# Performance work log

Measured on AMD Instinct MI355X. Metric: run time of the kernel, lower is better.

## Reference

```python
import jax, jax.numpy as jnp
import numpy as np

B, S, H, E, NF, NM = 4096, 512, 5, 4, 1, 64  # batch, seq, hidden, embed_dim, numeric feats, num_mote_ids
D = NF + E  # lstm input size = 5


def setup_inputs() -> dict:
    key = jax.random.key(0)
    k = jax.random.split(key, 7)
    s = 1.0 / np.sqrt(H)  # PyTorch LSTM init scale
    return {
        "x_num": jax.random.normal(k[0], (B, S, NF), jnp.float32),
        "x_cat": jax.random.randint(k[1], (B, S, 1), 0, NM, jnp.int32),
        "embed": jax.random.normal(k[2], (NM, E), jnp.float32),
        "W_ih": jax.random.uniform(k[3], (4 * H, D), jnp.float32, -s, s),
        "W_hh": jax.random.uniform(k[4], (4 * H, H), jnp.float32, -s, s),
        "b_ih": jax.random.uniform(k[5], (4 * H,), jnp.float32, -s, s),
        "b_hh": jax.random.uniform(k[6], (4 * H,), jnp.float32, -s, s),
    }


def reference(x_num, x_cat, embed, W_ih, W_hh, b_ih, b_hh):
    # embedding lookup + concat -> [B, S, D]
    emb = embed[x_cat[:, :, 0]]
    x = jnp.concatenate([x_num, emb], axis=2)
    # precompute input-to-gate projections once: [B, S, 4H]
    xg = jnp.einsum('bsd,gd->bsg', x, W_ih) + b_ih + b_hh

    def step(carry, xt):  # xt: [B, 4H]
        h, c = carry
        g = xt + h @ W_hh.T
        i, f, gg, o = jnp.split(g, 4, axis=-1)  # PyTorch gate order: i, f, g, o
        i = jax.nn.sigmoid(i)
        f = jax.nn.sigmoid(f)
        gg = jnp.tanh(gg)
        o = jax.nn.sigmoid(o)
        c = f * c + i * gg
        h = o * jnp.tanh(c)
        return (h, c), h

    h0 = jnp.zeros((B, H), x.dtype)
    c0 = jnp.zeros((B, H), x.dtype)
    (hT, cT), outs = jax.lax.scan(step, (h0, c0), jnp.swapaxes(xg, 0, 1))
    out = jnp.swapaxes(outs, 0, 1)  # [B, S, H]
    return out, hT[None], cT[None]  # hidden/cell: [num_layers=1, B, H]
```

## Files before the change

kernel.cpp:

```cpp
#include <hip/hip_runtime.h>

#define NBATCH 4096
#define SEQ 512
#define HID 5
#define NEMB 64

__device__ __forceinline__ float fexp2(float x){ return __builtin_amdgcn_exp2f(x); }
__device__ __forceinline__ float frcp(float x){ return __builtin_amdgcn_rcpf(x); }

#define SWZ(v, k) __int_as_float(__builtin_amdgcn_ds_swizzle(__float_as_int(v), ((4*(k)) << 5)))
#define DPPQ(v, j) __int_as_float(__builtin_amdgcn_update_dpp(0, __float_as_int(v), ((j) * 0x55), 0xF, 0xF, true))

__global__ __launch_bounds__(64) void lstm_enc_kernel(
    const float* __restrict__ x_num, const int* __restrict__ x_cat,
    const float* __restrict__ embed, const float* __restrict__ W_ih,
    const float* __restrict__ W_hh, const float* __restrict__ b_ih,
    const float* __restrict__ b_hh, float* __restrict__ out)
{
    __shared__ float4 s_emb[NEMB];
    int tid = threadIdx.x;
    s_emb[tid] = ((const float4*)embed)[tid];
    __syncthreads();

    int half = tid >> 5;
    int l    = tid & 31;
    int b    = blockIdx.x * 2 + half;
    int k    = ((l >> 2) < HID) ? (l >> 2) : (HID - 1);
    int g    = l & 3;
    bool st  = (l < 20) && (g == 0);

    const float L2E = 1.4426950408889634f;
    float s_  = (g == 2) ? (-2.0f * L2E) : (-L2E);
    float fm  = (g == 2) ? 2.0f : 1.0f;
    float fb  = (g == 2) ? -1.0f : 0.0f;

    int row = g * HID + k;
    float wi_[5], wh_[5];
#pragma unroll
    for (int d = 0; d < 5; ++d) {
        wi_[d] = W_ih[row * 5 + d] * s_;
        wh_[d] = W_hh[row * 5 + d] * s_;
    }
    float bias = (b_ih[row] + b_hh[row]) * s_;

    const float4* xp = (const float4*)(x_num + (size_t)b * SEQ);
    const int4*   cp = (const int4*)(x_cat + (size_t)b * SEQ);
    float* outp = out + (size_t)b * SEQ * HID + k;

    float h = 0.f, c = 0.f;
    float hb0 = 0.f, hb1 = 0.f, hb2 = 0.f, hb3 = 0.f, hb4 = 0.f;

    float4 xf = xp[0];
    int4   cf = cp[0];
    float4 ec_[4];
    ec_[0] = s_emb[cf.x]; ec_[1] = s_emb[cf.y];
    ec_[2] = s_emb[cf.z]; ec_[3] = s_emb[cf.w];

    for (int t0 = 0; t0 < SEQ; t0 += 4) {
        int nidx = (t0 + 4 < SEQ) ? ((t0 >> 2) + 1) : 0;
        float4 xf_n = xp[nidx];
        int4   cf_n = cp[nidx];

        float xn_a[4] = {xf.x, xf.y, xf.z, xf.w};

        float xa[4];
#pragma unroll
        for (int u = 0; u < 4; ++u) {
            float4 e = ec_[u];
            float a = fmaf(xn_a[u], wi_[0], bias);
            a = fmaf(e.x, wi_[1], a);
            a = fmaf(e.y, wi_[2], a);
            a = fmaf(e.z, wi_[3], a);
            a = fmaf(e.w, wi_[4], a);
            xa[u] = a;
        }

#pragma unroll
        for (int u = 0; u < 4; ++u) {
            float a = xa[u];
            a = fmaf(hb0, wh_[0], a);
            a = fmaf(hb1, wh_[1], a);
            a = fmaf(hb2, wh_[2], a);
            a = fmaf(hb3, wh_[3], a);
            a = fmaf(hb4, wh_[4], a);

            float r = frcp(1.0f + fexp2(a));
            float v = fmaf(r, fm, fb);

            float ai = DPPQ(v, 0);
            float af = DPPQ(v, 1);
            float ag = DPPQ(v, 2);
            float ao = DPPQ(v, 3);

            c = fmaf(af, c, ai * ag);
            float tc = fmaf(frcp(1.0f + fexp2(c * (-2.0f * L2E))), 2.0f, -1.0f);
            h = ao * tc;

            hb0 = SWZ(h, 0);
            hb1 = SWZ(h, 1);
            hb2 = SWZ(h, 2);
            hb3 = SWZ(h, 3);
            hb4 = SWZ(h, 4);

            if (st) outp[(t0 + u) * HID] = h;
        }

        ec_[0] = s_emb[cf_n.x]; ec_[1] = s_emb[cf_n.y];
        ec_[2] = s_emb[cf_n.z]; ec_[3] = s_emb[cf_n.w];
        xf = xf_n;
    }

    if (st) {
        size_t base = (size_t)NBATCH * SEQ * HID;
        out[base + (size_t)b * HID + k] = h;
        out[base + (size_t)NBATCH * HID + (size_t)b * HID + k] = c;
    }
}

extern "C" void kernel_launch(void* const* d_in, const int* in_sizes, int n_in,
                              void* d_out, int out_size, void* d_ws, size_t ws_size,
                              hipStream_t stream) {
    const float* x_num = (const float*)d_in[0];
    const int*   x_cat = (const int*)d_in[1];
    const float* embed = (const float*)d_in[2];
    const float* W_ih  = (const float*)d_in[3];
    const float* W_hh  = (const float*)d_in[4];
    const float* b_ih  = (const float*)d_in[5];
    const float* b_hh  = (const float*)d_in[6];
    float* out = (float*)d_out;

    dim3 grid(NBATCH / 2);
    dim3 block(64);
    hipLaunchKernelGGL(lstm_enc_kernel, grid, block, 0, stream,
                       x_num, x_cat, embed, W_ih, W_hh, b_ih, b_hh, out);
}
```

Before: 89.44 us.

## Interleave two independent batch recurrences per thread and halve the grid

Each wavefront now processes four batch sequences, two per half-wave, by running two independent LSTM recurrences interleaved in the same thread. The intent is to expose instruction-level parallelism across the latency-bound serial chain of cross-lane ops and exp/rcp, instead of relying on multiple waves per SIMD. The grid is halved, which reduces the number of resident waves, and register use roughly doubles.

After: 130.3 us. 1.46x slower.

```diff
diff --git a/kernel.cpp b/kernel.cpp
--- a/kernel.cpp
+++ b/kernel.cpp
@@ -24,7 +24,8 @@
 
     int half = tid >> 5;
     int l    = tid & 31;
-    int b    = blockIdx.x * 2 + half;
+    int bA   = blockIdx.x * 4 + half;
+    int bB   = bA + 2;
     int k    = ((l >> 2) < HID) ? (l >> 2) : (HID - 1);
     int g    = l & 3;
     bool st  = (l < 20) && (g == 0);
@@ -43,77 +44,111 @@
     }
     float bias = (b_ih[row] + b_hh[row]) * s_;
 
-    const float4* xp = (const float4*)(x_num + (size_t)b * SEQ);
-    const int4*   cp = (const int4*)(x_cat + (size_t)b * SEQ);
-    float* outp = out + (size_t)b * SEQ * HID + k;
+    const float4* xpA = (const float4*)(x_num + (size_t)bA * SEQ);
+    const int4*   cpA = (const int4*)(x_cat + (size_t)bA * SEQ);
+    float* outpA = out + (size_t)bA * SEQ * HID + k;
+    const float4* xpB = (const float4*)(x_num + (size_t)bB * SEQ);
+    const int4*   cpB = (const int4*)(x_cat + (size_t)bB * SEQ);
+    float* outpB = out + (size_t)bB * SEQ * HID + k;
 
-    float h = 0.f, c = 0.f;
-    float hb0 = 0.f, hb1 = 0.f, hb2 = 0.f, hb3 = 0.f, hb4 = 0.f;
+    float hA = 0.f, cA = 0.f, hB = 0.f, cB = 0.f;
+    float hbA0 = 0.f, hbA1 = 0.f, hbA2 = 0.f, hbA3 = 0.f, hbA4 = 0.f;
+    float hbB0 = 0.f, hbB1 = 0.f, hbB2 = 0.f, hbB3 = 0.f, hbB4 = 0.f;
 
-    float4 xf = xp[0];
-    int4   cf = cp[0];
-    float4 ec_[4];
-    ec_[0] = s_emb[cf.x]; ec_[1] = s_emb[cf.y];
-    ec_[2] = s_emb[cf.z]; ec_[3] = s_emb[cf.w];
+    float4 xfA = xpA[0];  int4 cfA = cpA[0];
+    float4 xfB = xpB[0];  int4 cfB = cpB[0];
+    float4 ecA_[4], ecB_[4];
+    ecA_[0] = s_emb[cfA.x]; ecA_[1] = s_emb[cfA.y]; ecA_[2] = s_emb[cfA.z]; ecA_[3] = s_emb[cfA.w];
+    ecB_[0] = s_emb[cfB.x]; ecB_[1] = s_emb[cfB.y]; ecB_[2] = s_emb[cfB.z]; ecB_[3] = s_emb[cfB.w];
 
     for (int t0 = 0; t0 < SEQ; t0 += 4) {
         int nidx = (t0 + 4 < SEQ) ? ((t0 >> 2) + 1) : 0;
-        float4 xf_n = xp[nidx];
-        int4   cf_n = cp[nidx];
+        float4 xfA_n = xpA[nidx];  int4 cfA_n = cpA[nidx];
+        float4 xfB_n = xpB[nidx];  int4 cfB_n = cpB[nidx];
 
-        float xn_a[4] = {xf.x, xf.y, xf.z, xf.w};
+        float xnA[4] = {xfA.x, xfA.y, xfA.z, xfA.w};
+        float xnB[4] = {xfB.x, xfB.y, xfB.z, xfB.w};
 
-        float xa[4];
+        float xaA[4], xaB[4];
 #pragma unroll
         for (int u = 0; u < 4; ++u) {
-            float4 e = ec_[u];
-            float a = fmaf(xn_a[u], wi_[0], bias);
-            a = fmaf(e.x, wi_[1], a);
-            a = fmaf(e.y, wi_[2], a);
-            a = fmaf(e.z, wi_[3], a);
-            a = fmaf(e.w, wi_[4], a);
-            xa[u] = a;
+            float4 eA = ecA_[u];
+            float a = fmaf(xnA[u], wi_[0], bias);
+            a = fmaf(eA.x, wi_[1], a);
+            a = fmaf(eA.y, wi_[2], a);
+            a = fmaf(eA.z, wi_[3], a);
+            a = fmaf(eA.w, wi_[4], a);
+            xaA[u] = a;
+            float4 eB = ecB_[u];
+            float bx = fmaf(xnB[u], wi_[0], bias);
+            bx = fmaf(eB.x, wi_[1], bx);
+            bx = fmaf(eB.y, wi_[2], bx);
+            bx = fmaf(eB.z, wi_[3], bx);
+            bx = fmaf(eB.w, wi_[4], bx);
+            xaB[u] = bx;
         }
 
 #pragma unroll
         for (int u = 0; u < 4; ++u) {
-            float a = xa[u];
-            a = fmaf(hb0, wh_[0], a);
-            a = fmaf(hb1, wh_[1], a);
-            a = fmaf(hb2, wh_[2], a);
-            a = fmaf(hb3, wh_[3], a);
-            a = fmaf(hb4, wh_[4], a);
-
-            float r = frcp(1.0f + fexp2(a));
-            float v = fmaf(r, fm, fb);
-
-            float ai = DPPQ(v, 0);
-            float af = DPPQ(v, 1);
-            float ag = DPPQ(v, 2);
-            float ao = DPPQ(v, 3);
-
-            c = fmaf(af, c, ai * ag);
-            float tc = fmaf(frcp(1.0f + fexp2(c * (-2.0f * L2E))), 2.0f, -1.0f);
-            h = ao * tc;
-
-            hb0 = SWZ(h, 0);
-            hb1 = SWZ(h, 1);
-            hb2 = SWZ(h, 2);
-            hb3 = SWZ(h, 3);
-            hb4 = SWZ(h, 4);
-
-            if (st) outp[(t0 + u) * HID] = h;
+            {
+                float a = xaA[u];
+                a = fmaf(hbA0, wh_[0], a);
+                a = fmaf(hbA1, wh_[1], a);
+                a = fmaf(hbA2, wh_[2], a);
+                a = fmaf(hbA3, wh_[3], a);
+                a = fmaf(hbA4, wh_[4], a);
+                float r = frcp(1.0f + fexp2(a));
+                float v = fmaf(r, fm, fb);
+                float ai = DPPQ(v, 0);
+                float af = DPPQ(v, 1);
+                float ag = DPPQ(v, 2);
+                float ao = DPPQ(v, 3);
+                cA = fmaf(af, cA, ai * ag);
+                float tc = fmaf(frcp(1.0f + fexp2(cA * (-2.0f * L2E))), 2.0f, -1.0f);
+                hA = ao * tc;
+                hbA0 = SWZ(hA, 0);
+                hbA1 = SWZ(hA, 1);
+                hbA2 = SWZ(hA, 2);
+                hbA3 = SWZ(hA, 3);
+                hbA4 = SWZ(hA, 4);
+                if (st) outpA[(t0 + u) * HID] = hA;
+            }
+            {
+                float a = xaB[u];
+                a = fmaf(hbB0, wh_[0], a);
+                a = fmaf(hbB1, wh_[1], a);
+                a = fmaf(hbB2, wh_[2], a);
+                a = fmaf(hbB3, wh_[3], a);
+                a = fmaf(hbB4, wh_[4], a);
+                float r = frcp(1.0f + fexp2(a));
+                float v = fmaf(r, fm, fb);
+                float ai = DPPQ(v, 0);
+                float af = DPPQ(v, 1);
+                float ag = DPPQ(v, 2);
+                float ao = DPPQ(v, 3);
+                cB = fmaf(af, cB, ai * ag);
+                float tc = fmaf(frcp(1.0f + fexp2(cB * (-2.0f * L2E))), 2.0f, -1.0f);
+                hB = ao * tc;
+                hbB0 = SWZ(hB, 0);
+                hbB1 = SWZ(hB, 1);
+                hbB2 = SWZ(hB, 2);
+                hbB3 = SWZ(hB, 3);
+                hbB4 = SWZ(hB, 4);
+                if (st) outpB[(t0 + u) * HID] = hB;
+            }
         }
 
-        ec_[0] = s_emb[cf_n.x]; ec_[1] = s_emb[cf_n.y];
-        ec_[2] = s_emb[cf_n.z]; ec_[3] = s_emb[cf_n.w];
-        xf = xf_n;
+        ecA_[0] = s_emb[cfA_n.x]; ecA_[1] = s_emb[cfA_n.y]; ecA_[2] = s_emb[cfA_n.z]; ecA_[3] = s_emb[cfA_n.w];
+        ecB_[0] = s_emb[cfB_n.x]; ecB_[1] = s_emb[cfB_n.y]; ecB_[2] = s_emb[cfB_n.z]; ecB_[3] = s_emb[cfB_n.w];
+        xfA = xfA_n; xfB = xfB_n;
     }
 
     if (st) {
         size_t base = (size_t)NBATCH * SEQ * HID;
-        out[base + (size_t)b * HID + k] = h;
-        out[base + (size_t)NBATCH * HID + (size_t)b * HID + k] = c;
+        out[base + (size_t)bA * HID + k] = hA;
+        out[base + (size_t)NBATCH * HID + (size_t)bA * HID + k] = cA;
+        out[base + (size_t)bB * HID + k] = hB;
+        out[base + (size_t)NBATCH * HID + (size_t)bB * HID + k] = cB;
     }
 }
 
@@ -129,7 +164,7 @@
     const float* b_hh  = (const float*)d_in[6];
     float* out = (float*)d_out;
 
-    dim3 grid(NBATCH / 2);
+    dim3 grid(NBATCH / 4);
     dim3 block(64);
     hipLaunchKernelGGL(lstm_enc_kernel, grid, block, 0, stream,
                        x_num, x_cat, embed, W_ih, W_hh, b_ih, b_hh, out);
```

## Pack four sequences per wave with 16-lane groups and DPP row rotations

Applied to the files above, without the earlier changes.

Each 64-lane wave now handles four batch sequences instead of two. Each 16-lane group computes gates for hidden units 0-3 in its lanes, and every lane also redundantly computes hidden unit 4. Cross-lane h broadcast now uses DPP row rotates instead of five ds_swizzle ops, which keeps the exchange in VALU rather than the LDS crossbar. Input prefetch is deepened to two chunks ahead, and the grid is halved. Each lane does roughly twice the serial ALU work, trading per-step latency for fewer idle lanes and fewer waves.

After: 97.32 us. 8.8% more time.

```diff
diff --git a/kernel.cpp b/kernel.cpp
--- a/kernel.cpp
+++ b/kernel.cpp
@@ -8,8 +8,11 @@
 __device__ __forceinline__ float fexp2(float x){ return __builtin_amdgcn_exp2f(x); }
 __device__ __forceinline__ float frcp(float x){ return __builtin_amdgcn_rcpf(x); }
 
-#define SWZ(v, k) __int_as_float(__builtin_amdgcn_ds_swizzle(__float_as_int(v), ((4*(k)) << 5)))
 #define DPPQ(v, j) __int_as_float(__builtin_amdgcn_update_dpp(0, __float_as_int(v), ((j) * 0x55), 0xF, 0xF, true))
+#define DPPZ(v, CTRL) __int_as_float(__builtin_amdgcn_update_dpp(0, __float_as_int(v), (CTRL), 0xF, 0xF, true))
+#define ROT4(v)  (DPPZ(v, 0x104) + DPPZ(v, 0x11C))
+#define ROT8(v)  (DPPZ(v, 0x128))
+#define ROT12(v) (DPPZ(v, 0x10C) + DPPZ(v, 0x114))
 
 __global__ __launch_bounds__(64) void lstm_enc_kernel(
     const float* __restrict__ x_num, const int* __restrict__ x_cat,
@@ -22,98 +25,119 @@
     s_emb[tid] = ((const float4*)embed)[tid];
     __syncthreads();
 
-    int half = tid >> 5;
-    int l    = tid & 31;
-    int b    = blockIdx.x * 2 + half;
-    int k    = ((l >> 2) < HID) ? (l >> 2) : (HID - 1);
-    int g    = l & 3;
-    bool st  = (l < 20) && (g == 0);
+    int grp = tid >> 4;
+    int l   = tid & 15;
+    int q   = l >> 2;
+    int g   = l & 3;
+    int b   = blockIdx.x * 4 + grp;
+
+    bool st  = (g == 0) || (l == 1);
+    bool is4 = (l == 1);
+    int  col = is4 ? 4 : q;
 
     const float L2E = 1.4426950408889634f;
-    float s_  = (g == 2) ? (-2.0f * L2E) : (-L2E);
+    const float CS  = -2.0f * L2E;
+    float s_  = (g == 2) ? CS : -L2E;
     float fm  = (g == 2) ? 2.0f : 1.0f;
     float fb  = (g == 2) ? -1.0f : 0.0f;
 
-    int row = g * HID + k;
-    float wi_[5], wh_[5];
+    int rowO = g * HID + q;
+    int row4 = g * HID + 4;
+    float wiO[5], wi4[5], wrO[5], wr4[5];
 #pragma unroll
     for (int d = 0; d < 5; ++d) {
-        wi_[d] = W_ih[row * 5 + d] * s_;
-        wh_[d] = W_hh[row * 5 + d] * s_;
+        wiO[d] = W_ih[rowO * 5 + d] * s_;
+        wi4[d] = W_ih[row4 * 5 + d] * s_;
     }
-    float bias = (b_ih[row] + b_hh[row]) * s_;
+#pragma unroll
+    for (int r = 0; r < 4; ++r) {
+        int idx = (q + r) & 3;
+        wrO[r] = W_hh[rowO * 5 + idx] * s_;
+        wr4[r] = W_hh[row4 * 5 + idx] * s_;
+    }
+    wrO[4] = W_hh[rowO * 5 + 4] * s_;
+    wr4[4] = W_hh[row4 * 5 + 4] * s_;
+    float biasO = (b_ih[rowO] + b_hh[rowO]) * s_;
+    float bias4 = (b_ih[row4] + b_hh[row4]) * s_;
 
     const float4* xp = (const float4*)(x_num + (size_t)b * SEQ);
     const int4*   cp = (const int4*)(x_cat + (size_t)b * SEQ);
-    float* outp = out + (size_t)b * SEQ * HID + k;
+    float* outp = out + (size_t)b * SEQ * HID;
 
-    float h = 0.f, c = 0.f;
-    float hb0 = 0.f, hb1 = 0.f, hb2 = 0.f, hb3 = 0.f, hb4 = 0.f;
+    float hq = 0.f, cq = 0.f, h4 = 0.f, c4 = 0.f;
 
-    float4 xf = xp[0];
-    int4   cf = cp[0];
-    float4 ec_[4];
-    ec_[0] = s_emb[cf.x]; ec_[1] = s_emb[cf.y];
-    ec_[2] = s_emb[cf.z]; ec_[3] = s_emb[cf.w];
+    float4 xf_c = xp[0];            int4 cf_c = cp[0];
+    float4 xf_1 = xp[1];            int4 cf_1 = cp[1];
+    float4 ec_c[4];
+    ec_c[0] = s_emb[cf_c.x]; ec_c[1] = s_emb[cf_c.y];
+    ec_c[2] = s_emb[cf_c.z]; ec_c[3] = s_emb[cf_c.w];
 
     for (int t0 = 0; t0 < SEQ; t0 += 4) {
-        int nidx = (t0 + 4 < SEQ) ? ((t0 >> 2) + 1) : 0;
-        float4 xf_n = xp[nidx];
-        int4   cf_n = cp[nidx];
+        int n2 = (t0 >> 2) + 2;
+        if (n2 > (SEQ / 4 - 1)) n2 = SEQ / 4 - 1;
+        float4 xf_2 = xp[n2];
+        int4   cf_2 = cp[n2];
 
-        float xn_a[4] = {xf.x, xf.y, xf.z, xf.w};
+        float4 ec_n0 = s_emb[cf_1.x];
+        float4 ec_n1 = s_emb[cf_1.y];
+        float4 ec_n2 = s_emb[cf_1.z];
+        float4 ec_n3 = s_emb[cf_1.w];
 
-        float xa[4];
+        float xn_a[4] = {xf_c.x, xf_c.y, xf_c.z, xf_c.w};
+
+        float xaO[4], xa4[4];
 #pragma unroll
         for (int u = 0; u < 4; ++u) {
-            float4 e = ec_[u];
-            float a = fmaf(xn_a[u], wi_[0], bias);
-            a = fmaf(e.x, wi_[1], a);
-            a = fmaf(e.y, wi_[2], a);
-            a = fmaf(e.z, wi_[3], a);
-            a = fmaf(e.w, wi_[4], a);
-            xa[u] = a;
+            float4 e = ec_c[u];
+            float aO = fmaf(xn_a[u], wiO[0], biasO);
+            float a4v = fmaf(xn_a[u], wi4[0], bias4);
+            aO  = fmaf(e.x, wiO[1], aO);   a4v = fmaf(e.x, wi4[1], a4v);
+            aO  = fmaf(e.y, wiO[2], aO);   a4v = fmaf(e.y, wi4[2], a4v);
+            aO  = fmaf(e.z, wiO[3], aO);   a4v = fmaf(e.z, wi4[3], a4v);
+            aO  = fmaf(e.w, wiO[4], aO);   a4v = fmaf(e.w, wi4[4], a4v);
+            xaO[u] = aO; xa4[u] = a4v;
         }
 
 #pragma unroll
         for (int u = 0; u < 4; ++u) {
-            float a = xa[u];
-            a = fmaf(hb0, wh_[0], a);
-            a = fmaf(hb1, wh_[1], a);
-            a = fmaf(hb2, wh_[2], a);
-            a = fmaf(hb3, wh_[3], a);
-            a = fmaf(hb4, wh_[4], a);
+            float aO = xaO[u], a4v = xa4[u];
+            aO = fmaf(h4, wrO[4], aO);   a4v = fmaf(h4, wr4[4], a4v);
+            aO = fmaf(hq, wrO[0], aO);   a4v = fmaf(hq, wr4[0], a4v);
+            float t4  = ROT4(hq);
+            float t8  = ROT8(hq);
+            float t12 = ROT12(hq);
+            aO = fmaf(t4,  wrO[1], aO);  a4v = fmaf(t4,  wr4[1], a4v);
+            aO = fmaf(t8,  wrO[2], aO);  a4v = fmaf(t8,  wr4[2], a4v);
+            aO = fmaf(t12, wrO[3], aO);  a4v = fmaf(t12, wr4[3], a4v);
 
-            float r = frcp(1.0f + fexp2(a));
-            float v = fmaf(r, fm, fb);
+            float rO = frcp(1.0f + fexp2(aO));
+            float r4 = frcp(1.0f + fexp2(a4v));
+            float vO = fmaf(rO, fm, fb);
+            float v4 = fmaf(r4, fm, fb);
 
-            float ai = DPPQ(v, 0);
-            float af = DPPQ(v, 1);
-            float ag = DPPQ(v, 2);
-            float ao = DPPQ(v, 3);
+            float aiO = DPPQ(vO, 0), afO = DPPQ(vO, 1), agO = DPPQ(vO, 2), aoO = DPPQ(vO, 3);
+            float ai4 = DPPQ(v4, 0), af4 = DPPQ(v4, 1), ag4 = DPPQ(v4, 2), ao4 = DPPQ(v4, 3);
 
-            c = fmaf(af, c, ai * ag);
-            float tc = fmaf(frcp(1.0f + fexp2(c * (-2.0f * L2E))), 2.0f, -1.0f);
-            h = ao * tc;
+            cq = fmaf(afO, cq, aiO * agO);
+            c4 = fmaf(af4, c4, ai4 * ag4);
 
-            hb0 = SWZ(h, 0);
-            hb1 = SWZ(h, 1);
-            hb2 = SWZ(h, 2);
-            hb3 = SWZ(h, 3);
-            hb4 = SWZ(h, 4);
+            float tO = frcp(1.0f + fexp2(cq * CS));
+            float t4c = frcp(1.0f + fexp2(c4 * CS));
+            hq = fmaf(tO,  aoO + aoO, -aoO);
+            h4 = fmaf(t4c, ao4 + ao4, -ao4);
 
-            if (st) outp[(t0 + u) * HID] = h;
+            if (st) outp[(t0 + u) * HID + col] = is4 ? h4 : hq;
         }
 
-        ec_[0] = s_emb[cf_n.x]; ec_[1] = s_emb[cf_n.y];
-        ec_[2] = s_emb[cf_n.z]; ec_[3] = s_emb[cf_n.w];
-        xf = xf_n;
+        ec_c[0] = ec_n0; ec_c[1] = ec_n1; ec_c[2] = ec_n2; ec_c[3] = ec_n3;
+        xf_c = xf_1; xf_1 = xf_2;
+        cf_c = cf_1; cf_1 = cf_2;
     }
 
     if (st) {
         size_t base = (size_t)NBATCH * SEQ * HID;
-        out[base + (size_t)b * HID + k] = h;
-        out[base + (size_t)NBATCH * HID + (size_t)b * HID + k] = c;
+        out[base + (size_t)b * HID + col] = is4 ? h4 : hq;
+        out[base + (size_t)NBATCH * HID + (size_t)b * HID + col] = is4 ? c4 : cq;
     }
 }
 
@@ -129,7 +153,7 @@
     const float* b_hh  = (const float*)d_in[6];
     float* out = (float*)d_out;
 
-    dim3 grid(NBATCH / 2);
+    dim3 grid(NBATCH / 4);
     dim3 block(64);
     hipLaunchKernelGGL(lstm_enc_kernel, grid, block, 0, stream,
                        x_num, x_cat, embed, W_ih, W_hh, b_ih, b_hh, out);
```
